# Performance work log

Measured on AMD Instinct MI355X. Metric: run time of the kernel, lower is better.

## Reference

```python
import jax, jax.numpy as jnp
import numpy as np

HIDDEN = 4096
N_HEADS = 32
N_KV_HEADS = 8
HEAD_DIM = HIDDEN // N_HEADS  # 128
KV_DIM = N_KV_HEADS * HEAD_DIM  # 1024
ROPE_THETA = 10000.0
B, S = 1, 2048


def setup_inputs() -> dict:
    key = jax.random.key(0)
    ks = jax.random.split(key, 5)
    scale = 0.02
    return {
        "positions": jnp.arange(B * S, dtype=jnp.int32).reshape(B, S),
        "hidden_states": jax.random.normal(ks[0], (B, S, HIDDEN), dtype=jnp.float32),
        "Wqkv": jax.random.normal(ks[1], (HIDDEN, HIDDEN + 2 * KV_DIM), dtype=jnp.float32) * scale,
        "bqkv": jax.random.normal(ks[2], (HIDDEN + 2 * KV_DIM,), dtype=jnp.float32) * scale,
        "Wproj": jax.random.normal(ks[3], (HIDDEN, HIDDEN), dtype=jnp.float32) * scale,
        "bproj": jax.random.normal(ks[4], (HIDDEN,), dtype=jnp.float32) * scale,
    }


def _apply_rope(x, positions):
    # x: [B, S, H, D]; NeoX-style rotation over full head_dim (vLLM get_rope default)
    half = HEAD_DIM // 2
    inv_freq = 1.0 / (ROPE_THETA ** (jnp.arange(0, half, dtype=jnp.float32) / half))
    angles = positions.astype(jnp.float32)[..., None] * inv_freq  # [B, S, half]
    cos = jnp.cos(angles)[:, :, None, :]  # [B, S, 1, half]
    sin = jnp.sin(angles)[:, :, None, :]
    x1, x2 = x[..., :half], x[..., half:]
    return jnp.concatenate([x1 * cos - x2 * sin, x2 * cos + x1 * sin], axis=-1)


def reference(positions, hidden_states, Wqkv, bqkv, Wproj, bproj):
    b, s, _ = hidden_states.shape
    qkv = hidden_states @ Wqkv + bqkv  # [B, S, HIDDEN + 2*KV_DIM]
    q, k, v = jnp.split(qkv, [HIDDEN, HIDDEN + KV_DIM], axis=-1)
    q = q.reshape(b, s, N_HEADS, HEAD_DIM)
    k = k.reshape(b, s, N_KV_HEADS, HEAD_DIM)
    v = v.reshape(b, s, N_KV_HEADS, HEAD_DIM)

    q = _apply_rope(q, positions)
    k = _apply_rope(k, positions)

    # GQA: expand kv heads to query heads (4 query heads per kv head)
    rep = N_HEADS // N_KV_HEADS
    k = jnp.repeat(k, rep, axis=2)  # [B, S, N_HEADS, D]
    v = jnp.repeat(v, rep, axis=2)

    scaling = 1.0 / np.sqrt(HEAD_DIM).astype(np.float32)
    scores = jnp.einsum("bqhd,bkhd->bhqk", q, k) * scaling  # [B, H, S, S]
    causal = jnp.tril(jnp.ones((s, s), dtype=bool))
    scores = jnp.where(causal[None, None], scores, jnp.finfo(scores.dtype).min)
    probs = jax.nn.softmax(scores, axis=-1)
    attn = jnp.einsum("bhqk,bkhd->bqhd", probs, v).reshape(b, s, HIDDEN)

    return attn @ Wproj + bproj
```

## Files before the change

### kernel.cpp

```cpp
#include <hip/hip_runtime.h>

#define HIDDEN 4096
#define NHEADS 32
#define NKV 8
#define HD 128
#define KVD 1024
#define QKVN 6144
#define SEQ 2048

typedef unsigned short u16;
typedef __bf16 bf16x8 __attribute__((ext_vector_type(8)));
typedef float f32x4 __attribute__((ext_vector_type(4)));
typedef unsigned short u16x4 __attribute__((ext_vector_type(4)));

__device__ __forceinline__ u16 f2b(float f) {
  union { float f; unsigned u; } v; v.f = f;
  unsigned r = (v.u + 0x7fffu + ((v.u >> 16) & 1u)) >> 16;
  return (u16)r;
}

__device__ __forceinline__ void gl_lds16(const void* g, void* l) {
  __builtin_amdgcn_global_load_lds(
      (const __attribute__((address_space(1))) unsigned*)g,
      (__attribute__((address_space(3))) unsigned*)l, 16, 0, 0);
}

__device__ __forceinline__ f32x4 mfma16(bf16x8 a, bf16x8 b, f32x4 c) {
  return __builtin_amdgcn_mfma_f32_16x16x32_bf16(a, b, c, 0, 0, 0);
}

__global__ void cvt_bf16(const float* __restrict__ x, u16* __restrict__ y, int n) {
  int i = (blockIdx.x * 256 + threadIdx.x) * 4;
  if (i < n) {
    float4 v = *(const float4*)(x + i);
    u16x4 o = {f2b(v.x), f2b(v.y), f2b(v.z), f2b(v.w)};
    *(u16x4*)(y + i) = o;
  }
}

__global__ void transpose_cvt64(const float* __restrict__ W, long ldW,
                                u16* __restrict__ Wt, long ldT) {
  __shared__ float tile[64][65];
  long c0 = blockIdx.x * 64L, r0 = blockIdx.y * 64L;
  int tx = threadIdx.x, ty = threadIdx.y;
#pragma unroll
  for (int i = 0; i < 4; ++i) {
    float4 v = *(const float4*)(W + (r0 + ty + i * 16) * ldW + c0 + tx * 4);
    tile[ty + i * 16][tx * 4 + 0] = v.x;
    tile[ty + i * 16][tx * 4 + 1] = v.y;
    tile[ty + i * 16][tx * 4 + 2] = v.z;
    tile[ty + i * 16][tx * 4 + 3] = v.w;
  }
  __syncthreads();
#pragma unroll
  for (int i = 0; i < 4; ++i) {
    int c = ty + i * 16;
    u16x4 o = {f2b(tile[tx * 4 + 0][c]), f2b(tile[tx * 4 + 1][c]),
               f2b(tile[tx * 4 + 2][c]), f2b(tile[tx * 4 + 3][c])};
    *(u16x4*)(Wt + (c0 + c) * ldT + r0 + tx * 4) = o;
  }
}

__global__ __launch_bounds__(256) void gemm_bt_bias(
    const u16* __restrict__ A, const u16* __restrict__ Bt,
    const float* __restrict__ bias, float* __restrict__ C,
    int M, int N, int K) {
  __shared__ u16 As[128 * 32];
  __shared__ u16 Bs[128 * 32];
  const int t = threadIdx.x;
  const int w = t >> 6, lane = t & 63, quad = lane >> 4, l15 = lane & 15;
  const int wy = w >> 1, wx = w & 1;
  const long m0 = blockIdx.y * 128L, n0 = blockIdx.x * 128L;
  f32x4 acc[4][4] = {};
  const u16* Ag = A + (m0 + (t >> 2)) * (long)K + (t & 3) * 8;
  const u16* Bg = Bt + (n0 + (t >> 2)) * (long)K + (t & 3) * 8;
  char* lA0 = (char*)As + w * 1024;
  char* lA1 = (char*)As + 4096 + w * 1024;
  char* lB0 = (char*)Bs + w * 1024;
  char* lB1 = (char*)Bs + 4096 + w * 1024;
  const long k64 = 64L * K;
  for (int k0 = 0; k0 < K; k0 += 32) {
    gl_lds16(Ag + k0, lA0);
    gl_lds16(Ag + k64 + k0, lA1);
    gl_lds16(Bg + k0, lB0);
    gl_lds16(Bg + k64 + k0, lB1);
    __syncthreads();
    bf16x8 af[4], bfr[4];
#pragma unroll
    for (int mi = 0; mi < 4; ++mi)
      af[mi] = *reinterpret_cast<const bf16x8*>(&As[(wy * 64 + mi * 16 + l15) * 32 + quad * 8]);
#pragma unroll
    for (int nj = 0; nj < 4; ++nj)
      bfr[nj] = *reinterpret_cast<const bf16x8*>(&Bs[(wx * 64 + nj * 16 + l15) * 32 + quad * 8]);
#pragma unroll
    for (int mi = 0; mi < 4; ++mi)
#pragma unroll
      for (int nj = 0; nj < 4; ++nj)
        acc[mi][nj] = mfma16(af[mi], bfr[nj], acc[mi][nj]);
    __syncthreads();
  }
#pragma unroll
  for (int mi = 0; mi < 4; ++mi) {
#pragma unroll
    for (int nj = 0; nj < 4; ++nj) {
      long n = n0 + wx * 64 + nj * 16 + l15;
      float bv = bias[n];
      long mrow = m0 + wy * 64 + mi * 16 + quad * 4;
#pragma unroll
      for (int r = 0; r < 4; ++r)
        C[(mrow + r) * (long)N + n] = acc[mi][nj][r] + bv;
    }
  }
}

__global__ __launch_bounds__(256) void gemm_qkv(
    const u16* __restrict__ A, const u16* __restrict__ Bt,
    const float* __restrict__ bias, const int* __restrict__ pos,
    u16* __restrict__ Qr, u16* __restrict__ Kr, u16* __restrict__ Vt) {
  __shared__ u16 As[128 * 32];
  __shared__ u16 Bs[128 * 32];
  const int K = HIDDEN;
  const int t = threadIdx.x;
  const int w = t >> 6, lane = t & 63, quad = lane >> 4, l15 = lane & 15;
  const long m0 = blockIdx.y * 128L, n0 = blockIdx.x * 128L;
  f32x4 acc[2][8] = {};
  const u16* Ag = A + (m0 + (t >> 2)) * (long)K + (t & 3) * 8;
  const u16* Bg = Bt + (n0 + (t >> 2)) * (long)K + (t & 3) * 8;
  char* lA0 = (char*)As + w * 1024;
  char* lA1 = (char*)As + 4096 + w * 1024;
  char* lB0 = (char*)Bs + w * 1024;
  char* lB1 = (char*)Bs + 4096 + w * 1024;
  const long k64 = 64L * K;
  for (int k0 = 0; k0 < K; k0 += 32) {
    gl_lds16(Ag + k0, lA0);
    gl_lds16(Ag + k64 + k0, lA1);
    gl_lds16(Bg + k0, lB0);
    gl_lds16(Bg + k64 + k0, lB1);
    __syncthreads();
    bf16x8 af[2], bfr[8];
#pragma unroll
    for (int mi = 0; mi < 2; ++mi)
      af[mi] = *reinterpret_cast<const bf16x8*>(&As[(w * 32 + mi * 16 + l15) * 32 + quad * 8]);
#pragma unroll
    for (int nj = 0; nj < 8; ++nj)
      bfr[nj] = *reinterpret_cast<const bf16x8*>(&Bs[(nj * 16 + l15) * 32 + quad * 8]);
#pragma unroll
    for (int mi = 0; mi < 2; ++mi)
#pragma unroll
      for (int nj = 0; nj < 8; ++nj)
        acc[mi][nj] = mfma16(af[mi], bfr[nj], acc[mi][nj]);
    __syncthreads();
  }

  const int tile = (int)(n0 >> 7);
  float bv[8];
#pragma unroll
  for (int nj = 0; nj < 8; ++nj) bv[nj] = bias[n0 + nj * 16 + l15];

  if (tile < 40) {
    const bool isQ = tile < 32;
    const float scq = 0.12751744154f;
    u16* outp = isQ ? (Qr + (long)tile * SEQ * HD)
                    : (Kr + (long)(tile - 32) * SEQ * HD);
    float invf[4];
#pragma unroll
    for (int nj = 0; nj < 4; ++nj) {
      float d = (float)(nj * 16 + l15);
      invf[nj] = __builtin_amdgcn_exp2f(-d * (13.287712379549449f / 64.0f));
    }
#pragma unroll
    for (int mi = 0; mi < 2; ++mi) {
#pragma unroll
      for (int r = 0; r < 4; ++r) {
        long s = m0 + w * 32 + mi * 16 + quad * 4 + r;
        float p = (float)pos[s];
        u16* rowp = outp + s * HD;
#pragma unroll
        for (int nj = 0; nj < 4; ++nj) {
          float ang = p * invf[nj];
          float cs, sn;
          __sincosf(ang, &sn, &cs);
          float x1 = acc[mi][nj][r] + bv[nj];
          float x2 = acc[mi][nj + 4][r] + bv[nj + 4];
          float o1 = x1 * cs - x2 * sn;
          float o2 = x2 * cs + x1 * sn;
          if (isQ) { o1 *= scq; o2 *= scq; }
          rowp[nj * 16 + l15] = f2b(o1);
          rowp[nj * 16 + l15 + 64] = f2b(o2);
        }
      }
    }
  } else {
    const int kvh = tile - 40;
    u16* outp = Vt + (long)kvh * HD * SEQ;
#pragma unroll
    for (int mi = 0; mi < 2; ++mi) {
      long s_base = m0 + w * 32 + mi * 16 + quad * 4;
#pragma unroll
      for (int nj = 0; nj < 8; ++nj) {
        int d = nj * 16 + l15;
        u16x4 o = {f2b(acc[mi][nj][0] + bv[nj]), f2b(acc[mi][nj][1] + bv[nj]),
                   f2b(acc[mi][nj][2] + bv[nj]), f2b(acc[mi][nj][3] + bv[nj])};
        *(u16x4*)(outp + (long)d * SEQ + s_base) = o;
      }
    }
  }
}

__device__ __forceinline__ void attn_tile(
    const bf16x8 q[4], const u16* KsF, const u16* VsF, u16* Psw,
    bool diag, int wq, int quad, int l15, f32x4 Oa[8], f32x4& lacc,
    bf16x8 ones) {
  f32x4 s[4] = {};
#pragma unroll
  for (int ks = 0; ks < 4; ++ks) {
#pragma unroll
    for (int nj = 0; nj < 4; ++nj) {
      bf16x8 bk = *reinterpret_cast<const bf16x8*>(
          &KsF[ks * 2048 + (nj * 16 + l15) * 32 + quad * 8]);
      s[nj] = mfma16(q[ks], bk, s[nj]);
    }
  }
#pragma unroll
  for (int nj = 0; nj < 4; ++nj) {
    int key = nj * 16 + l15;
    int ksw = key >> 5, kc = key & 31;
#pragma unroll
    for (int r = 0; r < 4; ++r) {
      float x = s[nj][r];
      if (diag && key > wq + r) x = -3.0e30f;
      Psw[ksw * 512 + (quad * 4 + r) * 32 + kc] = f2b(__builtin_amdgcn_exp2f(x));
    }
  }
#pragma unroll
  for (int ks = 0; ks < 2; ++ks) {
    bf16x8 ap = *reinterpret_cast<const bf16x8*>(&Psw[ks * 512 + l15 * 32 + quad * 8]);
    lacc = mfma16(ap, ones, lacc);
#pragma unroll
    for (int dj = 0; dj < 8; ++dj) {
      bf16x8 bv = *reinterpret_cast<const bf16x8*>(
          &VsF[ks * 4096 + (dj * 16 + l15) * 32 + quad * 8]);
      Oa[dj] = mfma16(ap, bv, Oa[dj]);
    }
  }
}

__global__ __launch_bounds__(256) void attn_fused(
    const u16* __restrict__ Qr, const u16* __restrict__ Kr,
    const u16* __restrict__ Vt, u16* __restrict__ Ao) {
  __shared__ u16 Ks[4 * 64 * 32];
  __shared__ u16 Vs[2 * 128 * 32];
  __shared__ u16 Ps[4][2 * 16 * 32];
  const int px = blockIdx.x, h = blockIdx.y, kvh = h >> 2;
  const int qtA = px, qtB = (SEQ / 64 - 1) - px;
  const int t = threadIdx.x, w = t >> 6, lane = t & 63;
  const int quad = lane >> 4, l15 = lane & 15;
  const int wq = w * 16 + quad * 4;
  u16* Psw = &Ps[w][0];

  bf16x8 ones;
  {
    union { u16 u[8]; bf16x8 v; } ou;
#pragma unroll
    for (int i = 0; i < 8; ++i) ou.u[i] = 0x3F80;
    ones = ou.v;
  }

  bf16x8 qA[4], qB[4];
  {
    const u16* QgA = Qr + ((long)h * SEQ + qtA * 64) * HD;
    const u16* QgB = Qr + ((long)h * SEQ + qtB * 64) * HD;
    long go = (long)(w * 16 + (lane >> 2)) * HD + (lane & 3) * 8;
#pragma unroll
    for (int j = 0; j < 4; ++j) {
      gl_lds16(QgA + go + j * 32, (char*)Ks + j * 4096 + w * 1024);
      gl_lds16(QgB + go + j * 32, (char*)Vs + j * 4096 + w * 1024);
    }
    __syncthreads();
#pragma unroll
    for (int j = 0; j < 4; ++j) {
      qA[j] = *reinterpret_cast<const bf16x8*>(&Ks[j * 2048 + (w * 16 + l15) * 32 + quad * 8]);
      qB[j] = *reinterpret_cast<const bf16x8*>(&Vs[j * 2048 + (w * 16 + l15) * 32 + quad * 8]);
    }
    __syncthreads();
  }

  f32x4 OaA[8] = {}, OaB[8] = {};
  f32x4 lA = {}, lB = {};
  const u16* Kg0 = Kr + (long)kvh * SEQ * HD;
  const u16* Vg0 = Vt + (long)kvh * HD * SEQ;

  for (int kt = 0; kt <= qtB; ++kt) {
    const int k0 = kt * 64;
    {
      const u16* Kg = Kg0 + (long)k0 * HD;
      long go = (long)(w * 16 + (lane >> 2)) * HD + (lane & 3) * 8;
#pragma unroll
      for (int j = 0; j < 4; ++j)
        gl_lds16(Kg + go + j * 32, (char*)Ks + j * 4096 + w * 1024);
      const u16* Vg = Vg0 + k0;
#pragma unroll
      for (int j = 0; j < 4; ++j) {
        int off = j * 2048 + w * 512 + lane * 8;
        int ks = off >> 12, rem = off & 4095;
        int dd = rem >> 5, kc = rem & 31;
        gl_lds16(Vg + (long)dd * SEQ + ks * 32 + kc, (char*)Vs + j * 4096 + w * 1024);
      }
    }
    __syncthreads();

    attn_tile(qB, Ks, Vs, Psw, kt == qtB, wq, quad, l15, OaB, lB, ones);
    if (kt <= qtA)
      attn_tile(qA, Ks, Vs, Psw, kt == qtA, wq, quad, l15, OaA, lA, ones);

    __syncthreads();
  }

#pragma unroll
  for (int r = 0; r < 4; ++r) {
    float invA = 1.0f / lA[r];
    float invB = 1.0f / lB[r];
    long rowA = (long)(qtA * 64 + w * 16 + quad * 4 + r) * HIDDEN + (long)h * HD;
    long rowB = (long)(qtB * 64 + w * 16 + quad * 4 + r) * HIDDEN + (long)h * HD;
#pragma unroll
    for (int dj = 0; dj < 8; ++dj) {
      Ao[rowA + dj * 16 + l15] = f2b(OaA[dj][r] * invA);
      Ao[rowB + dj * 16 + l15] = f2b(OaB[dj][r] * invB);
    }
  }
}

extern "C" void kernel_launch(void* const* d_in, const int* in_sizes, int n_in,
                              void* d_out, int out_size, void* d_ws, size_t ws_size,
                              hipStream_t stream) {
  const int* positions = (const int*)d_in[0];
  const float* hidden = (const float*)d_in[1];
  const float* Wqkv = (const float*)d_in[2];
  const float* bqkv = (const float*)d_in[3];
  const float* Wproj = (const float*)d_in[4];
  const float* bproj = (const float*)d_in[5];
  float* out = (float*)d_out;
  char* ws = (char*)d_ws;

  u16* Wqt = (u16*)(ws);
  u16* Wpt = (u16*)(ws + 50331648L);
  u16* Xb = (u16*)(ws + 83886080L);
  u16* Qr = (u16*)(ws + 100663296L);
  u16* Kr = (u16*)(ws + 117440512L);
  u16* Vt = (u16*)(ws + 121634816L);
  u16* Ao = (u16*)(ws + 125829120L);

  cvt_bf16<<<8192, 256, 0, stream>>>(hidden, Xb, SEQ * HIDDEN);
  transpose_cvt64<<<dim3(QKVN / 64, HIDDEN / 64), dim3(16, 16), 0, stream>>>(Wqkv, QKVN, Wqt, HIDDEN);
  transpose_cvt64<<<dim3(HIDDEN / 64, HIDDEN / 64), dim3(16, 16), 0, stream>>>(Wproj, HIDDEN, Wpt, HIDDEN);
  gemm_qkv<<<dim3(QKVN / 128, SEQ / 128), 256, 0, stream>>>(Xb, Wqt, bqkv, positions, Qr, Kr, Vt);
  attn_fused<<<dim3(SEQ / 128, NHEADS), 256, 0, stream>>>(Qr, Kr, Vt, Ao);
  gemm_bt_bias<<<dim3(HIDDEN / 128, SEQ / 128), 256, 0, stream>>>(Ao, Wpt, bproj, out, SEQ, HIDDEN, HIDDEN);
}
```

Measured before the change: 632.2 us.

## Split QKV GEMM epilogue into plain bf16 GEMM plus separate RoPE and V-transpose kernels

The fused QKV GEMM epilogue, which applied RoPE, Q scaling and the V transpose, is replaced by a generic bf16-output GEMM with a square 2x2 warp tiling. Two new kernels then apply RoPE to Q/K and transpose V into the layout the attention kernel expects. This simplifies the GEMM epilogue and changes its warp tiling, but adds an intermediate QKV buffer round-trip through global memory and two extra launches.

```diff
diff --git a/kernel.cpp b/kernel.cpp
--- a/kernel.cpp
+++ b/kernel.cpp
@@ -19,6 +19,11 @@
   return (u16)r;
 }
 
+__device__ __forceinline__ float b2f(u16 b) {
+  union { unsigned u; float f; } v; v.u = ((unsigned)b) << 16;
+  return v.f;
+}
+
 __device__ __forceinline__ void gl_lds16(const void* g, void* l) {
   __builtin_amdgcn_global_load_lds(
       (const __attribute__((address_space(1))) unsigned*)g,
@@ -50,6 +55,29 @@
     tile[ty + i * 16][tx * 4 + 1] = v.y;
     tile[ty + i * 16][tx * 4 + 2] = v.z;
     tile[ty + i * 16][tx * 4 + 3] = v.w;
+  }
+  __syncthreads();
+#pragma unroll
+  for (int i = 0; i < 4; ++i) {
+    int c = ty + i * 16;
+    u16x4 o = {f2b(tile[tx * 4 + 0][c]), f2b(tile[tx * 4 + 1][c]),
+               f2b(tile[tx * 4 + 2][c]), f2b(tile[tx * 4 + 3][c])};
+    *(u16x4*)(Wt + (c0 + c) * ldT + r0 + tx * 4) = o;
+  }
+}
+
+__global__ void transpose_b16(const u16* __restrict__ W, long ldW,
+                              u16* __restrict__ Wt, long ldT) {
+  __shared__ float tile[64][65];
+  long c0 = blockIdx.x * 64L, r0 = blockIdx.y * 64L;
+  int tx = threadIdx.x, ty = threadIdx.y;
+#pragma unroll
+  for (int i = 0; i < 4; ++i) {
+    u16x4 v = *(const u16x4*)(W + (r0 + ty + i * 16) * ldW + c0 + tx * 4);
+    tile[ty + i * 16][tx * 4 + 0] = b2f(v.x);
+    tile[ty + i * 16][tx * 4 + 1] = b2f(v.y);
+    tile[ty + i * 16][tx * 4 + 2] = b2f(v.z);
+    tile[ty + i * 16][tx * 4 + 3] = b2f(v.w);
   }
   __syncthreads();
 #pragma unroll
@@ -113,17 +141,17 @@
   }
 }
 
-__global__ __launch_bounds__(256) void gemm_qkv(
+__global__ __launch_bounds__(256) void gemm_bt_bias_b16(
     const u16* __restrict__ A, const u16* __restrict__ Bt,
-    const float* __restrict__ bias, const int* __restrict__ pos,
-    u16* __restrict__ Qr, u16* __restrict__ Kr, u16* __restrict__ Vt) {
+    const float* __restrict__ bias, u16* __restrict__ C,
+    int M, int N, int K) {
   __shared__ u16 As[128 * 32];
   __shared__ u16 Bs[128 * 32];
-  const int K = HIDDEN;
   const int t = threadIdx.x;
   const int w = t >> 6, lane = t & 63, quad = lane >> 4, l15 = lane & 15;
+  const int wy = w >> 1, wx = w & 1;
   const long m0 = blockIdx.y * 128L, n0 = blockIdx.x * 128L;
-  f32x4 acc[2][8] = {};
+  f32x4 acc[4][4] = {};
   const u16* Ag = A + (m0 + (t >> 2)) * (long)K + (t & 3) * 8;
   const u16* Bg = Bt + (n0 + (t >> 2)) * (long)K + (t & 3) * 8;
   char* lA0 = (char*)As + w * 1024;
@@ -137,73 +165,57 @@
     gl_lds16(Bg + k0, lB0);
     gl_lds16(Bg + k64 + k0, lB1);
     __syncthreads();
-    bf16x8 af[2], bfr[8];
-#pragma unroll
-    for (int mi = 0; mi < 2; ++mi)
-      af[mi] = *reinterpret_cast<const bf16x8*>(&As[(w * 32 + mi * 16 + l15) * 32 + quad * 8]);
-#pragma unroll
-    for (int nj = 0; nj < 8; ++nj)
-      bfr[nj] = *reinterpret_cast<const bf16x8*>(&Bs[(nj * 16 + l15) * 32 + quad * 8]);
-#pragma unroll
-    for (int mi = 0; mi < 2; ++mi)
-#pragma unroll
-      for (int nj = 0; nj < 8; ++nj)
+    bf16x8 af[4], bfr[4];
+#pragma unroll
+    for (int mi = 0; mi < 4; ++mi)
+      af[mi] = *reinterpret_cast<const bf16x8*>(&As[(wy * 64 + mi * 16 + l15) * 32 + quad * 8]);
+#pragma unroll
+    for (int nj = 0; nj < 4; ++nj)
+      bfr[nj] = *reinterpret_cast<const bf16x8*>(&Bs[(wx * 64 + nj * 16 + l15) * 32 + quad * 8]);
+#pragma unroll
+    for (int mi = 0; mi < 4; ++mi)
+#pragma unroll
+      for (int nj = 0; nj < 4; ++nj)
         acc[mi][nj] = mfma16(af[mi], bfr[nj], acc[mi][nj]);
     __syncthreads();
   }
-
-  const int tile = (int)(n0 >> 7);
-  float bv[8];
-#pragma unroll
-  for (int nj = 0; nj < 8; ++nj) bv[nj] = bias[n0 + nj * 16 + l15];
-
-  if (tile < 40) {
-    const bool isQ = tile < 32;
-    const float scq = 0.12751744154f;
-    u16* outp = isQ ? (Qr + (long)tile * SEQ * HD)
-                    : (Kr + (long)(tile - 32) * SEQ * HD);
-    float invf[4];
+#pragma unroll
+  for (int mi = 0; mi < 4; ++mi) {
 #pragma unroll
     for (int nj = 0; nj < 4; ++nj) {
-      float d = (float)(nj * 16 + l15);
-      invf[nj] = __builtin_amdgcn_exp2f(-d * (13.287712379549449f / 64.0f));
-    }
-#pragma unroll
-    for (int mi = 0; mi < 2; ++mi) {
-#pragma unroll
-      for (int r = 0; r < 4; ++r) {
-        long s = m0 + w * 32 + mi * 16 + quad * 4 + r;
-        float p = (float)pos[s];
-        u16* rowp = outp + s * HD;
-#pragma unroll
-        for (int nj = 0; nj < 4; ++nj) {
-          float ang = p * invf[nj];
-          float cs, sn;
-          __sincosf(ang, &sn, &cs);
-          float x1 = acc[mi][nj][r] + bv[nj];
-          float x2 = acc[mi][nj + 4][r] + bv[nj + 4];
-          float o1 = x1 * cs - x2 * sn;
-          float o2 = x2 * cs + x1 * sn;
-          if (isQ) { o1 *= scq; o2 *= scq; }
-          rowp[nj * 16 + l15] = f2b(o1);
-          rowp[nj * 16 + l15 + 64] = f2b(o2);
-        }
-      }
-    }
+      long n = n0 + wx * 64 + nj * 16 + l15;
+      float bv = bias[n];
+      long mrow = m0 + wy * 64 + mi * 16 + quad * 4;
+#pragma unroll
+      for (int r = 0; r < 4; ++r)
+        C[(mrow + r) * (long)N + n] = f2b(acc[mi][nj][r] + bv);
+    }
+  }
+}
+
+__global__ void rope_qk(const u16* __restrict__ qkv, const int* __restrict__ pos,
+                        u16* __restrict__ Qr, u16* __restrict__ Kr) {
+  int s = blockIdx.x;
+  int hl = threadIdx.x >> 6;
+  int d = threadIdx.x & 63;
+  int h = blockIdx.y * 4 + hl;
+  float p = (float)pos[s];
+  float inv = __builtin_amdgcn_exp2f(-(float)d * (13.287712379549449f / 64.0f));
+  float ang = p * inv;
+  float cs, sn;
+  __sincosf(ang, &sn, &cs);
+  long base = (long)s * QKVN + (long)h * HD;
+  float x1 = b2f(qkv[base + d]), x2 = b2f(qkv[base + d + 64]);
+  float o1 = x1 * cs - x2 * sn, o2 = x2 * cs + x1 * sn;
+  if (h < NHEADS) {
+    const float sc = 0.12751744154f;
+    long ob = ((long)h * SEQ + s) * HD;
+    Qr[ob + d] = f2b(o1 * sc);
+    Qr[ob + d + 64] = f2b(o2 * sc);
   } else {
-    const int kvh = tile - 40;
-    u16* outp = Vt + (long)kvh * HD * SEQ;
-#pragma unroll
-    for (int mi = 0; mi < 2; ++mi) {
-      long s_base = m0 + w * 32 + mi * 16 + quad * 4;
-#pragma unroll
-      for (int nj = 0; nj < 8; ++nj) {
-        int d = nj * 16 + l15;
-        u16x4 o = {f2b(acc[mi][nj][0] + bv[nj]), f2b(acc[mi][nj][1] + bv[nj]),
-                   f2b(acc[mi][nj][2] + bv[nj]), f2b(acc[mi][nj][3] + bv[nj])};
-        *(u16x4*)(outp + (long)d * SEQ + s_base) = o;
-      }
-    }
+    long ob = ((long)(h - NHEADS) * SEQ + s) * HD;
+    Kr[ob + d] = f2b(o1);
+    Kr[ob + d + 64] = f2b(o2);
   }
 }
 
@@ -345,15 +357,18 @@
   u16* Wqt = (u16*)(ws);
   u16* Wpt = (u16*)(ws + 50331648L);
   u16* Xb = (u16*)(ws + 83886080L);
-  u16* Qr = (u16*)(ws + 100663296L);
-  u16* Kr = (u16*)(ws + 117440512L);
-  u16* Vt = (u16*)(ws + 121634816L);
-  u16* Ao = (u16*)(ws + 125829120L);
+  u16* QKVb = (u16*)(ws + 100663296L);
+  u16* Qr = (u16*)(ws + 125829120L);
+  u16* Kr = (u16*)(ws + 142606336L);
+  u16* Vt = (u16*)(ws + 146800640L);
+  u16* Ao = (u16*)(ws + 150994944L);
 
   cvt_bf16<<<8192, 256, 0, stream>>>(hidden, Xb, SEQ * HIDDEN);
   transpose_cvt64<<<dim3(QKVN / 64, HIDDEN / 64), dim3(16, 16), 0, stream>>>(Wqkv, QKVN, Wqt, HIDDEN);
   transpose_cvt64<<<dim3(HIDDEN / 64, HIDDEN / 64), dim3(16, 16), 0, stream>>>(Wproj, HIDDEN, Wpt, HIDDEN);
-  gemm_qkv<<<dim3(QKVN / 128, SEQ / 128), 256, 0, stream>>>(Xb, Wqt, bqkv, positions, Qr, Kr, Vt);
+  gemm_bt_bias_b16<<<dim3(QKVN / 128, SEQ / 128), 256, 0, stream>>>(Xb, Wqt, bqkv, QKVb, SEQ, QKVN, HIDDEN);
+  rope_qk<<<dim3(SEQ, 10), 256, 0, stream>>>(QKVb, positions, Qr, Kr);
+  transpose_b16<<<dim3(KVD / 64, SEQ / 64), dim3(16, 16), 0, stream>>>(QKVb + 5120, QKVN, Vt, SEQ);
   attn_fused<<<dim3(SEQ / 128, NHEADS), 256, 0, stream>>>(Qr, Kr, Vt, Ao);
   gemm_bt_bias<<<dim3(HIDDEN / 128, SEQ / 128), 256, 0, stream>>>(Ao, Wpt, bproj, out, SEQ, HIDDEN, HIDDEN);
 }
```

Result: faster. 589.6 us (-6.7%).
